# Optimization experiments

Hardware: AMD Instinct MI355X
Metric: run time of the kernel (lower is better)

## Reference

```python
import jax, jax.numpy as jnp
import numpy as np

HEAD_SIZE = 64


def setup_inputs() -> dict:
    key = jax.random.key(0)
    k1, k2, k3, k4 = jax.random.split(key, 4)
    B, T, C, H = 8, 2048, 1024, HEAD_SIZE
    return {
        "idx": jax.random.normal(k1, (B, T, C), dtype=jnp.float32),
        "Wk": jax.random.normal(k2, (C, H), dtype=jnp.float32) * (C ** -0.5),
        "Wq": jax.random.normal(k3, (C, H), dtype=jnp.float32) * (C ** -0.5),
        "Wv": jax.random.normal(k4, (C, H), dtype=jnp.float32) * (C ** -0.5),
    }


def reference(idx, Wk, Wq, Wv):
    # idx: [B, T, C]; Wk/Wq/Wv: [C, H]
    B, T, C = idx.shape
    H = Wk.shape[1]
    k = idx @ Wk  # [B, T, H]
    q = idx @ Wq  # [B, T, H]
    v = idx @ Wv  # [B, T, H]
    # Faithful to source: wei = k @ q^T (note: k first, as written in the torch code)
    wei = jnp.einsum("bth,bsh->bts", k, q) * (H ** -0.5)  # [B, T, T]
    causal = jnp.tril(jnp.ones((T, T), dtype=bool))
    wei = jnp.where(causal, wei, -jnp.inf)
    wei = jax.nn.softmax(wei, axis=-1)
    # Dropout(0.5) treated as eval-mode identity (deterministic reference)
    out = jnp.einsum("bts,bsh->bth", wei, v)  # [B, T, H]
    return out
```

## Files before the change

### kernel.cpp

```cpp
#include <hip/hip_runtime.h>

#define B_ 8
#define T_ 2048
#define C_ 1024
#define H_ 64
#define BT_ (B_ * T_)

typedef float f32x4 __attribute__((ext_vector_type(4)));
typedef unsigned short u16x4 __attribute__((ext_vector_type(4)));
typedef unsigned short u16x8 __attribute__((ext_vector_type(8)));
typedef __bf16 bf16x8 __attribute__((ext_vector_type(8)));

static __device__ __forceinline__ unsigned short f2bf(float f) {
    unsigned int u = __builtin_bit_cast(unsigned int, f);
    u = (u + 0x7FFFu + ((u >> 16) & 1u)) >> 16;
    return (unsigned short)u;
}

static __device__ __forceinline__ f32x4 mfma16(u16x8 a, u16x8 b, f32x4 c) {
    return __builtin_amdgcn_mfma_f32_16x16x32_bf16(
        __builtin_bit_cast(bf16x8, a), __builtin_bit_cast(bf16x8, b), c, 0, 0, 0);
}

static __device__ __forceinline__ void cvtpk4(float a0, float a1, float a2, float a3,
                                              unsigned& d0, unsigned& d1) {
    asm("v_cvt_pk_bf16_f32 %0, %1, %2" : "=v"(d0) : "v"(a0), "v"(a1));
    asm("v_cvt_pk_bf16_f32 %0, %1, %2" : "=v"(d1) : "v"(a2), "v"(a3));
}

__global__ __launch_bounds__(256) void wprep(const float* __restrict__ Wk,
                                             const float* __restrict__ Wq,
                                             const float* __restrict__ Wv,
                                             unsigned short* __restrict__ wt) {
    __shared__ float tile[64][65];
    const int arr = blockIdx.x >> 4, ct = blockIdx.x & 15;
    const float* W = (arr == 0) ? Wk : ((arr == 1) ? Wq : Wv);
    const int tid = threadIdx.x;
    {
        int c = tid >> 2, seg = (tid & 3) << 4;
        const float* src = W + (size_t)(ct * 64 + c) * 64 + seg;
#pragma unroll
        for (int j = 0; j < 16; j += 4) {
            f32x4 v4 = *(const f32x4*)(src + j);
            tile[c][seg + j + 0] = v4[0];
            tile[c][seg + j + 1] = v4[1];
            tile[c][seg + j + 2] = v4[2];
            tile[c][seg + j + 3] = v4[3];
        }
    }
    __syncthreads();
    {
        int h = tid >> 2, cs = (tid & 3) << 4;
        unsigned short* dst = wt + (size_t)(arr * 64 + h) * 1024 + ct * 64 + cs;
#pragma unroll
        for (int j = 0; j < 16; ++j) dst[j] = f2bf(tile[cs + j][h]);
    }
}

__global__ __launch_bounds__(512, 4) void proj_gemm(const float* __restrict__ idx,
                                                    const unsigned short* __restrict__ wt,
                                                    unsigned short* __restrict__ kw,
                                                    unsigned short* __restrict__ qw,
                                                    unsigned short* __restrict__ vtw) {
    __shared__ unsigned short As[2][32 * 64];
    __shared__ unsigned short Bs[2][192 * 64];
    const int tid = threadIdx.x;
    const int lane = tid & 63, w = tid >> 6;
    const int g = lane >> 4, l15 = lane & 15;
    const int m0 = blockIdx.x * 32;
    const int arow = tid >> 4, aseg = tid & 15;

    f32x4 acc[3] = {};
    f32x4 areg;
    u16x8 breg[3];

    auto sload = [&](int k0) {
        areg = *(const f32x4*)(idx + (size_t)(m0 + arow) * 1024 + k0 + aseg * 4);
#pragma unroll
        for (int i = 0; i < 3; ++i) {
            int slot = i * 512 + tid, n = slot >> 3, u = slot & 7;
            breg[i] = *(const u16x8*)(wt + (size_t)n * 1024 + k0 + u * 8);
        }
    };
    auto swrite = [&](int buf) {
        unsigned d0, d1;
        cvtpk4(areg[0], areg[1], areg[2], areg[3], d0, d1);
        int au = aseg >> 1, ah = aseg & 1;
        uint2 pk; pk.x = d0; pk.y = d1;
        *(uint2*)&As[buf][arow * 64 + ((au ^ (arow & 7)) * 8) + ah * 4] = pk;
#pragma unroll
        for (int i = 0; i < 3; ++i) {
            int slot = i * 512 + tid, n = slot >> 3, u = slot & 7;
            *(u16x8*)&Bs[buf][n * 64 + ((u ^ (n & 7)) * 8)] = breg[i];
        }
    };

    sload(0);
    swrite(0);
    __syncthreads();

    int cur = 0;
    for (int kt = 0; kt < 16; ++kt) {
        if (kt < 15) sload((kt + 1) * 64);
#pragma unroll
        for (int ks = 0; ks < 2; ++ks) {
            u16x8 a = *(const u16x8*)&As[cur][((w & 1) * 16 + l15) * 64 +
                                              (((ks * 4 + g) ^ (l15 & 7)) * 8)];
#pragma unroll
            for (int nf = 0; nf < 3; ++nf) {
                int n = (w >> 1) * 48 + nf * 16 + l15;
                u16x8 b = *(const u16x8*)&Bs[cur][n * 64 + (((ks * 4 + g) ^ (n & 7)) * 8)];
                acc[nf] = mfma16(a, b, acc[nf]);
            }
        }
        if (kt < 15) swrite(cur ^ 1);
        __syncthreads();
        cur ^= 1;
    }

#pragma unroll
    for (int nf = 0; nf < 3; ++nf) {
        int nb = (w >> 1) * 3 + nf;
        int arr = nb >> 2;
        int nloc = ((nb & 3) << 4) + l15;
        f32x4 ac = acc[nf];
        int row = m0 + (w & 1) * 16 + g * 4;
        if (arr == 2) {
            u16x4 pk = {f2bf(ac[0]), f2bf(ac[1]), f2bf(ac[2]), f2bf(ac[3])};
            *(u16x4*)&vtw[(size_t)nloc * BT_ + row] = pk;
        } else {
            unsigned short* dst = arr ? qw : kw;
            dst[(size_t)(row + 0) * 64 + nloc] = f2bf(ac[0]);
            dst[(size_t)(row + 1) * 64 + nloc] = f2bf(ac[1]);
            dst[(size_t)(row + 2) * 64 + nloc] = f2bf(ac[2]);
            dst[(size_t)(row + 3) * 64 + nloc] = f2bf(ac[3]);
        }
    }
}

__global__ __launch_bounds__(512, 2) void attn_part(const unsigned short* __restrict__ kw,
                                                    const unsigned short* __restrict__ qw,
                                                    const unsigned short* __restrict__ vtw,
                                                    float* __restrict__ Opart,
                                                    float* __restrict__ lpart) {
    __shared__ unsigned short q_s[2][64 * 64];
    __shared__ unsigned short v_s[2][64 * 64];
    __shared__ unsigned short p_s[8 * 32 * 64];
    const int tid = threadIdx.x;
    const int w = tid >> 6, lane = tid & 63;
    const int g = lane >> 4, l15 = lane & 15;
    const int bid = blockIdx.x;
    const int b = bid & 7;
    const int rem = bid >> 3;
    const int j = rem & 7;
    const int part = rem >> 3;
    const size_t base = (size_t)b * T_;
    const int tA0 = 128 * j + 16 * w;
    const int tB0 = 128 * (15 - j) + 16 * w;
    const int nS = 2 * (16 - j);
    const int cnt = (nS - part + 3) >> 2;
    unsigned short* p_my = p_s + w * 2048;
    const float SCL = 0.125f * 1.44269504f;
    const float MOFF = 16.0f;
    const int sr = tid >> 3, su = tid & 7;

    u16x8 kf[2][2];
#pragma unroll
    for (int tf = 0; tf < 2; ++tf) {
        const unsigned short* kr = kw + (size_t)(base + (tf ? tB0 : tA0) + l15) * 64;
        kf[tf][0] = *(const u16x8*)(kr + g * 8);
        kf[tf][1] = *(const u16x8*)(kr + 32 + g * 8);
    }

    f32x4 o[4][2] = {};
    float l_lane[2] = {0.f, 0.f};

    u16x8 tq, tv;
    auto sload = [&](int st) {
        int s0 = st << 6;
        tq = *(const u16x8*)(qw + (size_t)(base + s0 + sr) * 64 + su * 8);
        tv = *(const u16x8*)(vtw + (size_t)sr * BT_ + base + s0 + su * 8);
    };
    auto swrite = [&](int buf) {
        *(u16x8*)&q_s[buf][sr * 64 + ((su ^ (sr & 7)) * 8)] = tq;
        *(u16x8*)&v_s[buf][sr * 64 + ((su ^ (sr & 7)) * 8)] = tv;
    };

    sload(part);
    swrite(0);
    __syncthreads();

    for (int i = 0; i < cnt; ++i) {
        const int st = part + 4 * i;
        const int s0 = st << 6;
        const int buf = i & 1;
        if (i + 1 < cnt) sload(part + 4 * (i + 1));
        const bool dA = (s0 <= tA0 + 15);
        const bool dB = (s0 <= tB0 + 15);

        u16x8 a[2][4];
#pragma unroll
        for (int ks = 0; ks < 2; ++ks)
#pragma unroll
            for (int sf = 0; sf < 4; ++sf)
                a[ks][sf] = *(const u16x8*)&q_s[buf][(sf * 16 + l15) * 64 +
                                                     (((ks * 4 + g) ^ (l15 & 7)) * 8)];

        f32x4 s_[4][2] = {};
        __builtin_amdgcn_s_setprio(1);
        if (dB) {
#pragma unroll
            for (int ks = 0; ks < 2; ++ks)
#pragma unroll
                for (int sf = 0; sf < 4; ++sf)
                    s_[sf][1] = mfma16(a[ks][sf], kf[1][ks], s_[sf][1]);
        }
        if (dA) {
#pragma unroll
            for (int ks = 0; ks < 2; ++ks)
#pragma unroll
                for (int sf = 0; sf < 4; ++sf)
                    s_[sf][0] = mfma16(a[ks][sf], kf[0][ks], s_[sf][0]);
        }
        __builtin_amdgcn_s_setprio(0);

#pragma unroll
        for (int tf_ = 1; tf_ >= 0; --tf_) {
            if (tf_ ? !dB : !dA) continue;
            const int tbase_ = tf_ ? tB0 : tA0;
            float pv[4][4];
#pragma unroll
            for (int sf = 0; sf < 4; ++sf)
#pragma unroll
                for (int r = 0; r < 4; ++r)
                    pv[sf][r] = exp2f(fmaf(s_[sf][tf_][r], SCL, -MOFF));
            if (s0 + 63 > tbase_) {
                const int t_ = tbase_ + l15;
#pragma unroll
                for (int sf = 0; sf < 4; ++sf)
#pragma unroll
                    for (int r = 0; r < 4; ++r) {
                        int sg = s0 + sf * 16 + g * 4 + r;
                        if (sg > t_) pv[sf][r] = 0.f;
                    }
            }
            float lacc = 0.f;
#pragma unroll
            for (int sf = 0; sf < 4; ++sf)
                lacc += (pv[sf][0] + pv[sf][1]) + (pv[sf][2] + pv[sf][3]);
            l_lane[tf_] += lacc;
            const int trow = tf_ * 16 + l15;
#pragma unroll
            for (int sf = 0; sf < 4; ++sf) {
                unsigned r0, r1;
                cvtpk4(pv[sf][0], pv[sf][1], pv[sf][2], pv[sf][3], r0, r1);
                int u16i = (sf * 2 + (g >> 1)) ^ (l15 & 7);
                uint2 pk; pk.x = r0; pk.y = r1;
                *(uint2*)&p_my[trow * 64 + u16i * 8 + (g & 1) * 4] = pk;
            }
        }

        u16x8 vf[2][4];
#pragma unroll
        for (int ks = 0; ks < 2; ++ks)
#pragma unroll
            for (int mf = 0; mf < 4; ++mf)
                vf[ks][mf] = *(const u16x8*)&v_s[buf][(mf * 16 + l15) * 64 +
                                                      (((ks * 4 + g) ^ (l15 & 7)) * 8)];
        __builtin_amdgcn_s_setprio(1);
#pragma unroll
        for (int ks = 0; ks < 2; ++ks) {
            if (dB) {
                u16x8 bp1 = *(const u16x8*)&p_my[(16 + l15) * 64 +
                                                 (((ks * 4 + g) ^ (l15 & 7)) * 8)];
#pragma unroll
                for (int mf = 0; mf < 4; ++mf)
                    o[mf][1] = mfma16(vf[ks][mf], bp1, o[mf][1]);
            }
            if (dA) {
                u16x8 bp0 = *(const u16x8*)&p_my[l15 * 64 +
                                                 (((ks * 4 + g) ^ (l15 & 7)) * 8)];
#pragma unroll
                for (int mf = 0; mf < 4; ++mf)
                    o[mf][0] = mfma16(vf[ks][mf], bp0, o[mf][0]);
            }
        }
        __builtin_amdgcn_s_setprio(0);

        if (i + 1 < cnt) swrite(buf ^ 1);
        __syncthreads();
    }

#pragma unroll
    for (int tf = 0; tf < 2; ++tf) {
        float ls = l_lane[tf];
        ls += __shfl_xor(ls, 16);
        ls += __shfl_xor(ls, 32);
        int rl = tf * 128 + w * 16 + l15;
        if (g == 0) lpart[(size_t)bid * 256 + rl] = ls;
#pragma unroll
        for (int mf = 0; mf < 4; ++mf)
            *(f32x4*)&Opart[(size_t)bid * 16384 + (size_t)rl * 64 + mf * 16 + g * 4] = o[mf][tf];
    }
}

__global__ __launch_bounds__(256) void attn_comb(const float* __restrict__ Opart,
                                                 const float* __restrict__ lpart,
                                                 float* __restrict__ out) {
    int gt = blockIdx.x * 256 + threadIdx.x;
    int row = gt >> 4;
    int h0 = (gt & 15) << 2;
    int b = row >> 11, t = row & 2047;
    int ti = t >> 7, rit = t & 127;
    int j = (ti < 8) ? ti : (15 - ti);
    int tf = (ti < 8) ? 0 : 1;
    int rl = tf * 128 + rit;
    f32x4 acc = {};
    float L = 0.f;
#pragma unroll
    for (int part = 0; part < 4; ++part) {
        int pb = b + 8 * j + 64 * part;
        acc += *(const f32x4*)&Opart[(size_t)pb * 16384 + (size_t)rl * 64 + h0];
        L += lpart[(size_t)pb * 256 + rl];
    }
    float inv = 1.f / L;
    *(f32x4*)&out[(size_t)row * 64 + h0] = acc * inv;
}

extern "C" void kernel_launch(void* const* d_in, const int* in_sizes, int n_in,
                              void* d_out, int out_size, void* d_ws, size_t ws_size,
                              hipStream_t stream) {
    const float* idx = (const float*)d_in[0];
    const float* Wk = (const float*)d_in[1];
    const float* Wq = (const float*)d_in[2];
    const float* Wv = (const float*)d_in[3];
    float* out = (float*)d_out;

    unsigned short* wt = (unsigned short*)d_ws;
    unsigned short* kw = wt + 192 * 1024;
    unsigned short* qw = kw + (size_t)BT_ * 64;
    unsigned short* vtw = qw + (size_t)BT_ * 64;
    float* Opart = (float*)((char*)d_ws + (8u << 20));
    float* lpart = Opart + (size_t)256 * 16384;

    wprep<<<48, 256, 0, stream>>>(Wk, Wq, Wv, wt);
    proj_gemm<<<512, 512, 0, stream>>>(idx, wt, kw, qw, vtw);
    attn_part<<<256, 512, 0, stream>>>(kw, qw, vtw, Opart, lpart);
    attn_comb<<<1024, 256, 0, stream>>>(Opart, lpart, out);
}
```

Before: 49.66 us.

## Rebalance attention split-K parts per row tile and double projection K-tile

The attention partial kernel now gives each query tile pair a variable number of split-K parts (5, 4 or 3, depending on how many key tiles it must cover) instead of a fixed 4. The total block count stays the same, and the goal is to even out the per-block work imbalance caused by causal masking. The combine kernel reads the matching variable number of partials. Separately, the projection GEMM K-tile grows from 64 to 128, halving the loop iterations and barriers. This roughly doubles its LDS use to about 112KB and lowers the occupancy hint from 4 to 2.

```diff
diff --git a/kernel.cpp b/kernel.cpp
--- a/kernel.cpp
+++ b/kernel.cpp
@@ -26,6 +26,13 @@
                                               unsigned& d0, unsigned& d1) {
     asm("v_cvt_pk_bf16_f32 %0, %1, %2" : "=v"(d0) : "v"(a0), "v"(a1));
     asm("v_cvt_pk_bf16_f32 %0, %1, %2" : "=v"(d1) : "v"(a2), "v"(a3));
+}
+
+static __device__ __forceinline__ int Pof(int j) {
+    return 5 - (j >= 2 ? 1 : 0) - (j >= 6 ? 1 : 0);
+}
+static __device__ __forceinline__ int offsof(int j) {
+    return (j < 2) ? 5 * j : (j < 6 ? 4 * j + 2 : 3 * j + 8);
 }
 
 __global__ __launch_bounds__(256) void wprep(const float* __restrict__ Wk,
@@ -57,13 +64,13 @@
     }
 }
 
-__global__ __launch_bounds__(512, 4) void proj_gemm(const float* __restrict__ idx,
+__global__ __launch_bounds__(512, 2) void proj_gemm(const float* __restrict__ idx,
                                                     const unsigned short* __restrict__ wt,
                                                     unsigned short* __restrict__ kw,
                                                     unsigned short* __restrict__ qw,
                                                     unsigned short* __restrict__ vtw) {
-    __shared__ unsigned short As[2][32 * 64];
-    __shared__ unsigned short Bs[2][192 * 64];
+    __shared__ unsigned short As[2][32 * 128];
+    __shared__ unsigned short Bs[2][192 * 128];
     const int tid = threadIdx.x;
     const int lane = tid & 63, w = tid >> 6;
     const int g = lane >> 4, l15 = lane & 15;
@@ -71,27 +78,29 @@
     const int arow = tid >> 4, aseg = tid & 15;
 
     f32x4 acc[3] = {};
-    f32x4 areg;
-    u16x8 breg[3];
+    f32x4 areg[2];
+    u16x8 breg[6];
 
     auto sload = [&](int k0) {
-        areg = *(const f32x4*)(idx + (size_t)(m0 + arow) * 1024 + k0 + aseg * 4);
-#pragma unroll
-        for (int i = 0; i < 3; ++i) {
-            int slot = i * 512 + tid, n = slot >> 3, u = slot & 7;
+        const float* src = idx + (size_t)(m0 + arow) * 1024 + k0 + aseg * 8;
+        areg[0] = ((const f32x4*)src)[0];
+        areg[1] = ((const f32x4*)src)[1];
+#pragma unroll
+        for (int i = 0; i < 6; ++i) {
+            int slot = i * 512 + tid, n = slot >> 4, u = slot & 15;
             breg[i] = *(const u16x8*)(wt + (size_t)n * 1024 + k0 + u * 8);
         }
     };
     auto swrite = [&](int buf) {
-        unsigned d0, d1;
-        cvtpk4(areg[0], areg[1], areg[2], areg[3], d0, d1);
-        int au = aseg >> 1, ah = aseg & 1;
-        uint2 pk; pk.x = d0; pk.y = d1;
-        *(uint2*)&As[buf][arow * 64 + ((au ^ (arow & 7)) * 8) + ah * 4] = pk;
-#pragma unroll
-        for (int i = 0; i < 3; ++i) {
-            int slot = i * 512 + tid, n = slot >> 3, u = slot & 7;
-            *(u16x8*)&Bs[buf][n * 64 + ((u ^ (n & 7)) * 8)] = breg[i];
+        unsigned d0, d1, d2, d3;
+        cvtpk4(areg[0][0], areg[0][1], areg[0][2], areg[0][3], d0, d1);
+        cvtpk4(areg[1][0], areg[1][1], areg[1][2], areg[1][3], d2, d3);
+        uint4 pk; pk.x = d0; pk.y = d1; pk.z = d2; pk.w = d3;
+        *(uint4*)&As[buf][arow * 128 + ((aseg ^ (arow & 7)) * 8)] = pk;
+#pragma unroll
+        for (int i = 0; i < 6; ++i) {
+            int slot = i * 512 + tid, n = slot >> 4, u = slot & 15;
+            *(u16x8*)&Bs[buf][n * 128 + ((u ^ (n & 7)) * 8)] = breg[i];
         }
     };
 
@@ -100,20 +109,20 @@
     __syncthreads();
 
     int cur = 0;
-    for (int kt = 0; kt < 16; ++kt) {
-        if (kt < 15) sload((kt + 1) * 64);
-#pragma unroll
-        for (int ks = 0; ks < 2; ++ks) {
-            u16x8 a = *(const u16x8*)&As[cur][((w & 1) * 16 + l15) * 64 +
+    for (int kt = 0; kt < 8; ++kt) {
+        if (kt < 7) sload((kt + 1) * 128);
+#pragma unroll
+        for (int ks = 0; ks < 4; ++ks) {
+            u16x8 a = *(const u16x8*)&As[cur][((w & 1) * 16 + l15) * 128 +
                                               (((ks * 4 + g) ^ (l15 & 7)) * 8)];
 #pragma unroll
             for (int nf = 0; nf < 3; ++nf) {
                 int n = (w >> 1) * 48 + nf * 16 + l15;
-                u16x8 b = *(const u16x8*)&Bs[cur][n * 64 + (((ks * 4 + g) ^ (n & 7)) * 8)];
+                u16x8 b = *(const u16x8*)&Bs[cur][n * 128 + (((ks * 4 + g) ^ (n & 7)) * 8)];
                 acc[nf] = mfma16(a, b, acc[nf]);
             }
         }
-        if (kt < 15) swrite(cur ^ 1);
+        if (kt < 7) swrite(cur ^ 1);
         __syncthreads();
         cur ^= 1;
     }
@@ -152,13 +161,13 @@
     const int bid = blockIdx.x;
     const int b = bid & 7;
     const int rem = bid >> 3;
-    const int j = rem & 7;
-    const int part = rem >> 3;
+    const int j = (rem < 10) ? (rem / 5) : (rem < 26 ? (rem - 2) >> 2 : (rem - 8) / 3);
+    const int P = Pof(j);
+    const int part = rem - offsof(j);
     const size_t base = (size_t)b * T_;
     const int tA0 = 128 * j + 16 * w;
     const int tB0 = 128 * (15 - j) + 16 * w;
     const int nS = 2 * (16 - j);
-    const int cnt = (nS - part + 3) >> 2;
     unsigned short* p_my = p_s + w * 2048;
     const float SCL = 0.125f * 1.44269504f;
     const float MOFF = 16.0f;
@@ -190,11 +199,12 @@
     swrite(0);
     __syncthreads();
 
-    for (int i = 0; i < cnt; ++i) {
-        const int st = part + 4 * i;
+    int i = 0;
+    for (int st = part; st < nS; st += P, ++i) {
         const int s0 = st << 6;
         const int buf = i & 1;
-        if (i + 1 < cnt) sload(part + 4 * (i + 1));
+        const bool more = (st + P < nS);
+        if (more) sload(st + P);
         const bool dA = (s0 <= tA0 + 15);
         const bool dB = (s0 <= tB0 + 15);
 
@@ -287,7 +297,7 @@
         }
         __builtin_amdgcn_s_setprio(0);
 
-        if (i + 1 < cnt) swrite(buf ^ 1);
+        if (more) swrite(buf ^ 1);
         __syncthreads();
     }
 
@@ -315,11 +325,11 @@
     int j = (ti < 8) ? ti : (15 - ti);
     int tf = (ti < 8) ? 0 : 1;
     int rl = tf * 128 + rit;
+    int P = Pof(j), offs = offsof(j);
     f32x4 acc = {};
     float L = 0.f;
-#pragma unroll
-    for (int part = 0; part < 4; ++part) {
-        int pb = b + 8 * j + 64 * part;
+    for (int p = 0; p < P; ++p) {
+        int pb = b + 8 * (offs + p);
         acc += *(const f32x4*)&Opart[(size_t)pb * 16384 + (size_t)rl * 64 + h0];
         L += lpart[(size_t)pb * 256 + rl];
     }
```

New measurement: 58.10 us. +17.0%, slower.

## Rebalance attention split-K parts per row tile and deepen projection prefetch

Applied to the files above, without the earlier changes.

The attention partial kernel now gives each row-tile pair j a variable number of key-range parts (5, 4 or 3) instead of a fixed 4. Pairs with more causal key tiles get more blocks, which evens out per-block work and shortens the tail; the combine kernel reads the matching variable number of partials. The projection GEMM now keeps two register sets of prefetched A/B tiles, issuing global loads two k-steps ahead to hide memory latency. The extra prefetch set costs more registers, which may reduce occupancy.

```diff
diff --git a/kernel.cpp b/kernel.cpp
--- a/kernel.cpp
+++ b/kernel.cpp
@@ -26,6 +26,13 @@
                                               unsigned& d0, unsigned& d1) {
     asm("v_cvt_pk_bf16_f32 %0, %1, %2" : "=v"(d0) : "v"(a0), "v"(a1));
     asm("v_cvt_pk_bf16_f32 %0, %1, %2" : "=v"(d1) : "v"(a2), "v"(a3));
+}
+
+static __device__ __forceinline__ int Pof(int j) {
+    return 5 - (j >= 2 ? 1 : 0) - (j >= 6 ? 1 : 0);
+}
+static __device__ __forceinline__ int offsof(int j) {
+    return (j < 2) ? 5 * j : (j < 6 ? 4 * j + 2 : 3 * j + 8);
 }
 
 __global__ __launch_bounds__(256) void wprep(const float* __restrict__ Wk,
@@ -71,37 +78,38 @@
     const int arow = tid >> 4, aseg = tid & 15;
 
     f32x4 acc[3] = {};
-    f32x4 areg;
-    u16x8 breg[3];
-
-    auto sload = [&](int k0) {
-        areg = *(const f32x4*)(idx + (size_t)(m0 + arow) * 1024 + k0 + aseg * 4);
+    f32x4 areg[2];
+    u16x8 breg[2][3];
+
+    auto sload = [&](int set, int k0) {
+        areg[set] = *(const f32x4*)(idx + (size_t)(m0 + arow) * 1024 + k0 + aseg * 4);
 #pragma unroll
         for (int i = 0; i < 3; ++i) {
             int slot = i * 512 + tid, n = slot >> 3, u = slot & 7;
-            breg[i] = *(const u16x8*)(wt + (size_t)n * 1024 + k0 + u * 8);
+            breg[set][i] = *(const u16x8*)(wt + (size_t)n * 1024 + k0 + u * 8);
         }
     };
-    auto swrite = [&](int buf) {
+    auto swrite = [&](int set, int buf) {
         unsigned d0, d1;
-        cvtpk4(areg[0], areg[1], areg[2], areg[3], d0, d1);
+        cvtpk4(areg[set][0], areg[set][1], areg[set][2], areg[set][3], d0, d1);
         int au = aseg >> 1, ah = aseg & 1;
         uint2 pk; pk.x = d0; pk.y = d1;
         *(uint2*)&As[buf][arow * 64 + ((au ^ (arow & 7)) * 8) + ah * 4] = pk;
 #pragma unroll
         for (int i = 0; i < 3; ++i) {
             int slot = i * 512 + tid, n = slot >> 3, u = slot & 7;
-            *(u16x8*)&Bs[buf][n * 64 + ((u ^ (n & 7)) * 8)] = breg[i];
+            *(u16x8*)&Bs[buf][n * 64 + ((u ^ (n & 7)) * 8)] = breg[set][i];
         }
     };
 
-    sload(0);
-    swrite(0);
+    sload(0, 0);
+    sload(1, 64);
+    swrite(0, 0);
     __syncthreads();
 
-    int cur = 0;
     for (int kt = 0; kt < 16; ++kt) {
-        if (kt < 15) sload((kt + 1) * 64);
+        const int cur = kt & 1;
+        if (kt < 14) sload(cur, (kt + 2) * 64);
 #pragma unroll
         for (int ks = 0; ks < 2; ++ks) {
             u16x8 a = *(const u16x8*)&As[cur][((w & 1) * 16 + l15) * 64 +
@@ -113,9 +121,8 @@
                 acc[nf] = mfma16(a, b, acc[nf]);
             }
         }
-        if (kt < 15) swrite(cur ^ 1);
+        if (kt < 15) swrite(cur ^ 1, cur ^ 1);
         __syncthreads();
-        cur ^= 1;
     }
 
 #pragma unroll
@@ -152,13 +159,13 @@
     const int bid = blockIdx.x;
     const int b = bid & 7;
     const int rem = bid >> 3;
-    const int j = rem & 7;
-    const int part = rem >> 3;
+    const int j = (rem < 10) ? (rem / 5) : (rem < 26 ? (rem - 2) >> 2 : (rem - 8) / 3);
+    const int P = Pof(j);
+    const int part = rem - offsof(j);
     const size_t base = (size_t)b * T_;
     const int tA0 = 128 * j + 16 * w;
     const int tB0 = 128 * (15 - j) + 16 * w;
     const int nS = 2 * (16 - j);
-    const int cnt = (nS - part + 3) >> 2;
     unsigned short* p_my = p_s + w * 2048;
     const float SCL = 0.125f * 1.44269504f;
     const float MOFF = 16.0f;
@@ -190,11 +197,12 @@
     swrite(0);
     __syncthreads();
 
-    for (int i = 0; i < cnt; ++i) {
-        const int st = part + 4 * i;
+    int i = 0;
+    for (int st = part; st < nS; st += P, ++i) {
         const int s0 = st << 6;
         const int buf = i & 1;
-        if (i + 1 < cnt) sload(part + 4 * (i + 1));
+        const bool more = (st + P < nS);
+        if (more) sload(st + P);
         const bool dA = (s0 <= tA0 + 15);
         const bool dB = (s0 <= tB0 + 15);
 
@@ -287,7 +295,7 @@
         }
         __builtin_amdgcn_s_setprio(0);
 
-        if (i + 1 < cnt) swrite(buf ^ 1);
+        if (more) swrite(buf ^ 1);
         __syncthreads();
     }
 
@@ -315,11 +323,11 @@
     int j = (ti < 8) ? ti : (15 - ti);
     int tf = (ti < 8) ? 0 : 1;
     int rl = tf * 128 + rit;
+    int P = Pof(j), offs = offsof(j);
     f32x4 acc = {};
     float L = 0.f;
-#pragma unroll
-    for (int part = 0; part < 4; ++part) {
-        int pb = b + 8 * j + 64 * part;
+    for (int p = 0; p < P; ++p) {
+        int pb = b + 8 * (offs + p);
         acc += *(const f32x4*)&Opart[(size_t)pb * 16384 + (size_t)rl * 64 + h0];
         L += lpart[(size_t)pb * 256 + rl];
     }
```

After: 50.72 us. 1.02x slower.
